# Performance work log

Measured on AMD Instinct MI355X. Metric: run time of the kernel, lower is better.

The kernel has to match this reference:

```python
import jax, jax.numpy as jnp
import numpy as np

N_NODES = 50000
N_EDGES = 800000
D_IN, D_HID, D_OUT = 128, 256, 128


def setup_inputs() -> dict:
    key = jax.random.key(0)
    ks = jax.random.split(key, 8)
    x = jax.random.normal(ks[0], (N_NODES, D_IN), dtype=jnp.float32)
    edge_index = jax.random.randint(ks[1], (2, N_EDGES), 0, N_NODES, dtype=jnp.int64)
    # Xavier-ish scale for stability
    W_l1 = jax.random.normal(ks[2], (D_HID, D_IN), dtype=jnp.float32) * (1.0 / np.sqrt(D_IN))
    b_l1 = jnp.zeros((D_HID,), dtype=jnp.float32)
    W_r1 = jax.random.normal(ks[3], (D_HID, D_IN), dtype=jnp.float32) * (1.0 / np.sqrt(D_IN))
    W_l2 = jax.random.normal(ks[4], (D_OUT, D_HID), dtype=jnp.float32) * (1.0 / np.sqrt(D_HID))
    b_l2 = jnp.zeros((D_OUT,), dtype=jnp.float32)
    W_r2 = jax.random.normal(ks[5], (D_OUT, D_HID), dtype=jnp.float32) * (1.0 / np.sqrt(D_HID))
    return {"x": x, "edge_index": edge_index, "W_l1": W_l1, "b_l1": b_l1,
            "W_r1": W_r1, "W_l2": W_l2, "b_l2": b_l2, "W_r2": W_r2}


def _sage_conv(x, src, dst, W_l, b_l, W_r):
    # SAGEConv (aggr='mean', root_weight=True, normalize=False):
    #   out_i = W_l @ mean_{j in N(i)} x_j + b_l + W_r @ x_i
    n = x.shape[0]
    msgs = x[src]                                             # [E, d] gather
    agg = jax.ops.segment_sum(msgs, dst, num_segments=n)      # [N, d] scatter-add
    deg = jax.ops.segment_sum(jnp.ones((src.shape[0],), x.dtype), dst,
                              num_segments=n)
    agg = agg / jnp.maximum(deg, 1.0)[:, None]                # mean (0 for isolated)
    return agg @ W_l.T + b_l + x @ W_r.T


def reference(x, edge_index, W_l1, b_l1, W_r1, W_l2, b_l2, W_r2):
    # Note: PyG BasicGNN with num_layers=1 and jk=None applies NO activation
    # after its single conv, so the stack is two bare SAGEConv layers.
    src, dst = edge_index[0], edge_index[1]
    h = _sage_conv(x, src, dst, W_l1, b_l1, W_r1)
    out = _sage_conv(h, src, dst, W_l2, b_l2, W_r2)
    return out
```

## Files before the change

kernel.cpp:

```cpp
#include <hip/hip_runtime.h>

typedef __attribute__((ext_vector_type(4))) float f32x4;
typedef __attribute__((ext_vector_type(8))) short bf16x8;

__device__ inline ushort f2bf(float f) {
    uint u = __builtin_bit_cast(uint, f);
    u += 0x7fff + ((u >> 16) & 1);
    return (ushort)(u >> 16);
}
__device__ inline float bf2f(ushort h) {
    uint u = ((uint)h) << 16;
    return __builtin_bit_cast(float, u);
}

#define GRP 8
#define NSLICE 6250
#define CHUNK 2048

__global__ __launch_bounds__(256) void k_hist_p(const int* __restrict__ ei,
                                                int* __restrict__ cnt, int nE) {
    const int g = blockIdx.x & 7;
    const int c = blockIdx.x >> 3;
    const int lo = g * NSLICE, hi = lo + NSLICE;
    #pragma unroll
    for (int p = 0; p < CHUNK / 256; ++p) {
        int e = c * CHUNK + p * 256 + threadIdx.x;
        if (e < nE) {
            int d = ei[nE + e];
            if (d >= lo && d < hi) atomicAdd(&cnt[d], 1);
        }
    }
}

__global__ __launch_bounds__(1024) void k_scan1(const int* __restrict__ cnt,
                                                int* __restrict__ rp,
                                                int* __restrict__ bsum, int n) {
    __shared__ int buf[1024];
    const int tid = threadIdx.x;
    const int i = blockIdx.x * 1024 + tid;
    int v = (i < n) ? cnt[i] : 0;
    buf[tid] = v;
    __syncthreads();
    #pragma unroll
    for (int off = 1; off < 1024; off <<= 1) {
        int t = 0;
        if (tid >= off) t = buf[tid - off];
        __syncthreads();
        if (tid >= off) buf[tid] += t;
        __syncthreads();
    }
    if (i < n) rp[i] = buf[tid] - v;
    if (tid == 1023) bsum[blockIdx.x] = buf[1023];
}

__global__ void k_scan2(const int* __restrict__ bsum, int* __restrict__ bofs,
                        int* __restrict__ rp, int nb, int n) {
    if (threadIdx.x == 0 && blockIdx.x == 0) {
        int run = 0;
        for (int b = 0; b < nb; ++b) { bofs[b] = run; run += bsum[b]; }
        rp[n] = run;
    }
}

__global__ __launch_bounds__(1024) void k_scan3(int* __restrict__ rp,
                                                const int* __restrict__ bofs, int n) {
    int i = blockIdx.x * 1024 + threadIdx.x;
    if (i < n) rp[i] += bofs[blockIdx.x];
}

__global__ __launch_bounds__(256) void k_fill_p(const int* __restrict__ ei,
                                                const int* __restrict__ rp,
                                                int* __restrict__ cur,
                                                int* __restrict__ srt, int nE) {
    const int g = blockIdx.x & 7;
    const int c = blockIdx.x >> 3;
    const int lo = g * NSLICE, hi = lo + NSLICE;
    #pragma unroll
    for (int p = 0; p < CHUNK / 256; ++p) {
        int e = c * CHUNK + p * 256 + threadIdx.x;
        if (e < nE) {
            int d = ei[nE + e];
            int s = ei[e];
            if (d >= lo && d < hi) {
                int pos = rp[d] + atomicAdd(&cur[d], 1);
                srt[pos] = s;
            }
        }
    }
}

__global__ __launch_bounds__(256) void k_cvt_x(const float* __restrict__ x,
                                               ushort* __restrict__ A1, int n) {
    int e4 = blockIdx.x * 256 + threadIdx.x;
    if (e4 >= n * 32) return;
    int i = e4 >> 5, c4 = e4 & 31;
    float4 v = *(const float4*)(x + (size_t)i * 128 + c4 * 4);
    ushort4 o;
    o.x = f2bf(v.x); o.y = f2bf(v.y); o.z = f2bf(v.z); o.w = f2bf(v.w);
    *(ushort4*)(A1 + (size_t)i * 256 + 128 + c4 * 4) = o;
}

__global__ __launch_bounds__(256) void k_cvt_w(
    const float* __restrict__ Wl1, const float* __restrict__ Wr1,
    const float* __restrict__ Wl2, const float* __restrict__ Wr2,
    ushort* __restrict__ W1cat, ushort* __restrict__ W2cat) {
    int t = blockIdx.x * 256 + threadIdx.x;
    int which = t >> 14;
    int r = (t >> 6) & 255;
    int kq = t & 63;
    const float* src;
    ushort* dst;
    if (which == 0) {
        src = (kq < 32) ? (Wl1 + (size_t)r * 128 + kq * 4)
                        : (Wr1 + (size_t)r * 128 + (kq - 32) * 4);
        dst = W1cat + (size_t)r * 256 + kq * 4;
    } else {
        src = (r < 128) ? (Wl2 + (size_t)r * 256 + kq * 4)
                        : (Wr2 + (size_t)(r - 128) * 256 + kq * 4);
        dst = W2cat + (size_t)r * 256 + kq * 4;
    }
    float4 v = *(const float4*)src;
    ushort4 o;
    o.x = f2bf(v.x); o.y = f2bf(v.y); o.z = f2bf(v.z); o.w = f2bf(v.w);
    *(ushort4*)dst = o;
}

__global__ __launch_bounds__(256) void k_gather1(ushort* A1,
                                                 const int* __restrict__ srt,
                                                 const int* __restrict__ rp, int n) {
    const int node = blockIdx.x * 4 + (threadIdx.x >> 6);
    if (node >= n) return;
    const int lane = threadIdx.x & 63;
    const int beg = rp[node], end = rp[node + 1];
    float ax = 0.f, ay = 0.f;
    int e = beg;
    for (; e + 7 < end; e += 8) {
        uint v[8];
        #pragma unroll
        for (int q = 0; q < 8; ++q)
            v[q] = *(const uint*)(A1 + (size_t)srt[e + q] * 256 + 128 + lane * 2);
        #pragma unroll
        for (int q = 0; q < 8; ++q) {
            ax += bf2f((ushort)v[q]);
            ay += bf2f((ushort)(v[q] >> 16));
        }
    }
    for (; e < end; ++e) {
        uint v0 = *(const uint*)(A1 + (size_t)srt[e] * 256 + 128 + lane * 2);
        ax += bf2f((ushort)v0);
        ay += bf2f((ushort)(v0 >> 16));
    }
    const float invd = 1.0f / fmaxf((float)(end - beg), 1.0f);
    uint o = ((uint)f2bf(ay * invd) << 16) | (uint)f2bf(ax * invd);
    *(uint*)(A1 + (size_t)node * 256 + lane * 2) = o;
}

__global__ __launch_bounds__(256) void k_gather2(const ushort* __restrict__ H2,
                                                 const int* __restrict__ srt,
                                                 const int* __restrict__ rp,
                                                 const float* __restrict__ b2,
                                                 float* __restrict__ out, int n) {
    const int node = blockIdx.x * 4 + (threadIdx.x >> 6);
    if (node >= n) return;
    const int lane = threadIdx.x & 63;
    const int beg = rp[node], end = rp[node + 1];
    float ax = 0.f, ay = 0.f;
    int e = beg;
    for (; e + 7 < end; e += 8) {
        uint v[8];
        #pragma unroll
        for (int q = 0; q < 8; ++q)
            v[q] = *(const uint*)(H2 + (size_t)srt[e + q] * 256 + lane * 2);
        #pragma unroll
        for (int q = 0; q < 8; ++q) {
            ax += bf2f((ushort)v[q]);
            ay += bf2f((ushort)(v[q] >> 16));
        }
    }
    for (; e < end; ++e) {
        uint v0 = *(const uint*)(H2 + (size_t)srt[e] * 256 + lane * 2);
        ax += bf2f((ushort)v0);
        ay += bf2f((ushort)(v0 >> 16));
    }
    const float invd = 1.0f / fmaxf((float)(end - beg), 1.0f);
    uint rv = *(const uint*)(H2 + (size_t)node * 256 + 128 + lane * 2);
    float2 bb = *(const float2*)(b2 + lane * 2);
    float2 res;
    res.x = ax * invd + bf2f((ushort)rv) + bb.x;
    res.y = ay * invd + bf2f((ushort)(rv >> 16)) + bb.y;
    *(float2*)(out + (size_t)node * 128 + lane * 2) = res;
}

__global__ __launch_bounds__(512, 4) void k_gemm_fused(
    const ushort* __restrict__ A, const ushort* __restrict__ W1,
    const ushort* __restrict__ W2, const float* __restrict__ b1,
    ushort* __restrict__ O, int n)
{
    __shared__ __align__(16) char sA[32768];
    __shared__ __align__(16) char sH[32768];
    const int bi = blockIdx.x * 64;
    const int tid = threadIdx.x;

    #pragma unroll
    for (int p = 0; p < 4; ++p) {
        const int o = p * 8192 + tid * 16;
        const int row = o >> 9;
        const int cb = o & 511;
        uint4 v = *(const uint4*)((const char*)A + (size_t)(bi + row) * 512 + cb);
        *(uint4*)(sA + row * 512 + (cb ^ ((row & 7) << 4))) = v;
    }
    __syncthreads();

    const int wid = tid >> 6;
    const int lane = tid & 63;
    const int wn = wid * 32;
    const int lr = lane & 15;
    const int lkb = (lane >> 4) * 16;
    const int crow0 = (lane >> 4) * 4;
    const int ccol = lane & 15;

    {
        f32x4 acc[4][2] = {};
        #pragma unroll
        for (int kk = 0; kk < 8; ++kk) {
            bf16x8 wf[2], af[4];
            #pragma unroll
            for (int ni = 0; ni < 2; ++ni)
                wf[ni] = *(const bf16x8*)((const char*)W1 + (size_t)(wn + ni * 16 + lr) * 512 + kk * 64 + lkb);
            #pragma unroll
            for (int mi = 0; mi < 4; ++mi) {
                const int row = mi * 16 + lr;
                af[mi] = *(const bf16x8*)(sA + row * 512 + ((kk * 64 + lkb) ^ ((row & 7) << 4)));
            }
            #pragma unroll
            for (int mi = 0; mi < 4; ++mi)
                #pragma unroll
                for (int ni = 0; ni < 2; ++ni)
                    acc[mi][ni] = __builtin_amdgcn_mfma_f32_16x16x32_bf16(
                        af[mi], wf[ni], acc[mi][ni], 0, 0, 0);
        }
        const float badd0 = b1[wn + ccol];
        const float badd1 = b1[wn + 16 + ccol];
        #pragma unroll
        for (int mi = 0; mi < 4; ++mi)
            #pragma unroll
            for (int ni = 0; ni < 2; ++ni) {
                const int col = wn + ni * 16 + ccol;
                const float badd = ni ? badd1 : badd0;
                #pragma unroll
                for (int j = 0; j < 4; ++j) {
                    const int row = mi * 16 + crow0 + j;
                    *(ushort*)(sH + row * 512 + ((col * 2) ^ ((row & 7) << 4))) =
                        f2bf(acc[mi][ni][j] + badd);
                }
            }
    }
    __syncthreads();

    {
        f32x4 acc[4][2] = {};
        #pragma unroll
        for (int kk = 0; kk < 8; ++kk) {
            bf16x8 wf[2], af[4];
            #pragma unroll
            for (int ni = 0; ni < 2; ++ni)
                wf[ni] = *(const bf16x8*)((const char*)W2 + (size_t)(wn + ni * 16 + lr) * 512 + kk * 64 + lkb);
            #pragma unroll
            for (int mi = 0; mi < 4; ++mi) {
                const int row = mi * 16 + lr;
                af[mi] = *(const bf16x8*)(sH + row * 512 + ((kk * 64 + lkb) ^ ((row & 7) << 4)));
            }
            #pragma unroll
            for (int mi = 0; mi < 4; ++mi)
                #pragma unroll
                for (int ni = 0; ni < 2; ++ni)
                    acc[mi][ni] = __builtin_amdgcn_mfma_f32_16x16x32_bf16(
                        af[mi], wf[ni], acc[mi][ni], 0, 0, 0);
        }
        #pragma unroll
        for (int mi = 0; mi < 4; ++mi)
            #pragma unroll
            for (int ni = 0; ni < 2; ++ni) {
                const int ocol = wn + ni * 16 + ccol;
                #pragma unroll
                for (int j = 0; j < 4; ++j) {
                    const int grow = bi + mi * 16 + crow0 + j;
                    if (grow < n)
                        O[(size_t)grow * 256 + ocol] = f2bf(acc[mi][ni][j]);
                }
            }
    }
}

extern "C" void kernel_launch(void* const* d_in, const int* in_sizes, int n_in,
                              void* d_out, int out_size, void* d_ws, size_t ws_size,
                              hipStream_t stream) {
    const float* x   = (const float*)d_in[0];
    const int*   ei  = (const int*)  d_in[1];
    const float* Wl1 = (const float*)d_in[2];
    const float* bl1 = (const float*)d_in[3];
    const float* Wr1 = (const float*)d_in[4];
    const float* Wl2 = (const float*)d_in[5];
    const float* bl2 = (const float*)d_in[6];
    const float* Wr2 = (const float*)d_in[7];
    float* out = (float*)d_out;

    const int nN = 50000;
    const int nE = in_sizes[1] / 2;

    char* ws = (char*)d_ws;
    int*    rp    = (int*)   (ws);
    int*    cnt   = (int*)   (ws + 262144);
    int*    cur   = (int*)   (ws + 524288);
    int*    bsum  = (int*)   (ws + 786432);
    int*    bofs  = (int*)   (ws + 790528);
    int*    srt   = (int*)   (ws + (size_t)1 * (1 << 20));
    ushort* W1cat = (ushort*)(ws + (size_t)5 * (1 << 20));
    ushort* W2cat = (ushort*)(ws + (size_t)5 * (1 << 20) + 256 * 1024);
    ushort* A1    = (ushort*)(ws + (size_t)6 * (1 << 20));
    ushort* H2    = (ushort*)(ws + (size_t)32 * (1 << 20));

    const int nb = (nN + 1023) / 1024;
    const int nChunks = (nE + CHUNK - 1) / CHUNK;

    hipMemsetAsync(ws + 262144, 0, 462144, stream);
    k_hist_p<<<nChunks * GRP, 256, 0, stream>>>(ei, cnt, nE);
    k_scan1<<<nb, 1024, 0, stream>>>(cnt, rp, bsum, nN);
    k_scan2<<<1, 64, 0, stream>>>(bsum, bofs, rp, nb, nN);
    k_scan3<<<nb, 1024, 0, stream>>>(rp, bofs, nN);
    k_fill_p<<<nChunks * GRP, 256, 0, stream>>>(ei, rp, cur, srt, nE);

    k_cvt_x<<<(nN * 32 + 255) / 256, 256, 0, stream>>>(x, A1, nN);
    k_cvt_w<<<128, 256, 0, stream>>>(Wl1, Wr1, Wl2, Wr2, W1cat, W2cat);

    k_gather1<<<(nN + 3) / 4, 256, 0, stream>>>(A1, srt, rp, nN);
    k_gemm_fused<<<(nN + 63) / 64, 512, 0, stream>>>(A1, W1cat, W2cat, bl1, H2, nN);

    k_gather2<<<(nN + 3) / 4, 256, 0, stream>>>(H2, srt, rp, bl2, out, nN);
}
```

Baseline: 294.5 us.

## Bucket CSR edges by source slice and gather 8 nodes per wave in lockstep

Splits each destination's neighbor list into 8 sub-buckets keyed by source-node slice, so the CSR is built over N*8 keys. The gather kernels then process 8 destination nodes per wavefront and walk all of them through the same source slice together. The goal is better L2 locality for the random row gathers and more loads in flight per wave. It also parallelizes the block-sum scan across a wavefront and merges the two conversion kernels into one launch. The cost is an 8x larger count/scan array, extra scan work, and divergent per-node loops inside each wave.

```diff
diff --git a/kernel.cpp b/kernel.cpp
--- a/kernel.cpp
+++ b/kernel.cpp
@@ -18,7 +18,7 @@
 #define CHUNK 2048
 
 __global__ __launch_bounds__(256) void k_hist_p(const int* __restrict__ ei,
-                                                int* __restrict__ cnt, int nE) {
+                                                int* __restrict__ cnt8, int nE) {
     const int g = blockIdx.x & 7;
     const int c = blockIdx.x >> 3;
     const int lo = g * NSLICE, hi = lo + NSLICE;
@@ -27,7 +27,8 @@
         int e = c * CHUNK + p * 256 + threadIdx.x;
         if (e < nE) {
             int d = ei[nE + e];
-            if (d >= lo && d < hi) atomicAdd(&cnt[d], 1);
+            int s = ei[e];
+            if (d >= lo && d < hi) atomicAdd(&cnt8[d * 8 + s / NSLICE], 1);
         }
     }
 }
@@ -55,11 +56,21 @@
 
 __global__ void k_scan2(const int* __restrict__ bsum, int* __restrict__ bofs,
                         int* __restrict__ rp, int nb, int n) {
-    if (threadIdx.x == 0 && blockIdx.x == 0) {
-        int run = 0;
-        for (int b = 0; b < nb; ++b) { bofs[b] = run; run += bsum[b]; }
-        rp[n] = run;
-    }
+    const int lane = threadIdx.x & 63;
+    int carry = 0;
+    for (int c = 0; c * 64 < nb; ++c) {
+        int i = c * 64 + lane;
+        int v = (i < nb) ? bsum[i] : 0;
+        int s = v;
+        #pragma unroll
+        for (int off = 1; off < 64; off <<= 1) {
+            int t = __shfl_up(s, off, 64);
+            if (lane >= off) s += t;
+        }
+        if (i < nb) bofs[i] = carry + s - v;
+        carry += __shfl(s, 63, 64);
+    }
+    if (lane == 0) rp[n] = carry;
 }
 
 __global__ __launch_bounds__(1024) void k_scan3(int* __restrict__ rp,
@@ -69,8 +80,8 @@
 }
 
 __global__ __launch_bounds__(256) void k_fill_p(const int* __restrict__ ei,
-                                                const int* __restrict__ rp,
-                                                int* __restrict__ cur,
+                                                const int* __restrict__ rp8,
+                                                int* __restrict__ cur8,
                                                 int* __restrict__ srt, int nE) {
     const int g = blockIdx.x & 7;
     const int c = blockIdx.x >> 3;
@@ -82,29 +93,34 @@
             int d = ei[nE + e];
             int s = ei[e];
             if (d >= lo && d < hi) {
-                int pos = rp[d] + atomicAdd(&cur[d], 1);
+                int k = d * 8 + s / NSLICE;
+                int pos = rp8[k] + atomicAdd(&cur8[k], 1);
                 srt[pos] = s;
             }
         }
     }
 }
 
-__global__ __launch_bounds__(256) void k_cvt_x(const float* __restrict__ x,
-                                               ushort* __restrict__ A1, int n) {
-    int e4 = blockIdx.x * 256 + threadIdx.x;
-    if (e4 >= n * 32) return;
-    int i = e4 >> 5, c4 = e4 & 31;
-    float4 v = *(const float4*)(x + (size_t)i * 128 + c4 * 4);
-    ushort4 o;
-    o.x = f2bf(v.x); o.y = f2bf(v.y); o.z = f2bf(v.z); o.w = f2bf(v.w);
-    *(ushort4*)(A1 + (size_t)i * 256 + 128 + c4 * 4) = o;
-}
-
-__global__ __launch_bounds__(256) void k_cvt_w(
-    const float* __restrict__ Wl1, const float* __restrict__ Wr1,
-    const float* __restrict__ Wl2, const float* __restrict__ Wr2,
-    ushort* __restrict__ W1cat, ushort* __restrict__ W2cat) {
-    int t = blockIdx.x * 256 + threadIdx.x;
+__global__ __launch_bounds__(256) void k_cvt(const float* __restrict__ x,
+                                             const float* __restrict__ Wl1,
+                                             const float* __restrict__ Wr1,
+                                             const float* __restrict__ Wl2,
+                                             const float* __restrict__ Wr2,
+                                             ushort* __restrict__ A1,
+                                             ushort* __restrict__ W1cat,
+                                             ushort* __restrict__ W2cat, int n) {
+    const int nxb = (n * 32 + 255) / 256;
+    if (blockIdx.x < nxb) {
+        int e4 = blockIdx.x * 256 + threadIdx.x;
+        if (e4 >= n * 32) return;
+        int i = e4 >> 5, c4 = e4 & 31;
+        float4 v = *(const float4*)(x + (size_t)i * 128 + c4 * 4);
+        ushort4 o;
+        o.x = f2bf(v.x); o.y = f2bf(v.y); o.z = f2bf(v.z); o.w = f2bf(v.w);
+        *(ushort4*)(A1 + (size_t)i * 256 + 128 + c4 * 4) = o;
+        return;
+    }
+    int t = (blockIdx.x - nxb) * 256 + threadIdx.x;
     int which = t >> 14;
     int r = (t >> 6) & 255;
     int kq = t & 63;
@@ -127,68 +143,114 @@
 
 __global__ __launch_bounds__(256) void k_gather1(ushort* A1,
                                                  const int* __restrict__ srt,
-                                                 const int* __restrict__ rp, int n) {
-    const int node = blockIdx.x * 4 + (threadIdx.x >> 6);
-    if (node >= n) return;
+                                                 const int* __restrict__ rp8, int n) {
+    const int wav = blockIdx.x * 4 + (threadIdx.x >> 6);
+    const int base = wav * 8;
+    if (base >= n) return;
     const int lane = threadIdx.x & 63;
-    const int beg = rp[node], end = rp[node + 1];
-    float ax = 0.f, ay = 0.f;
-    int e = beg;
-    for (; e + 7 < end; e += 8) {
-        uint v[8];
-        #pragma unroll
-        for (int q = 0; q < 8; ++q)
-            v[q] = *(const uint*)(A1 + (size_t)srt[e + q] * 256 + 128 + lane * 2);
+    float ax[8] = {}, ay[8] = {};
+    int deg[8] = {};
+    int curq[8], endq[8];
+    #pragma unroll
+    for (int q = 0; q < 8; ++q)
+        curq[q] = (base + q < n) ? rp8[(base + q) * 8] : 0;
+
+    #pragma unroll
+    for (int p = 0; p < 8; ++p) {
         #pragma unroll
         for (int q = 0; q < 8; ++q) {
-            ax += bf2f((ushort)v[q]);
-            ay += bf2f((ushort)(v[q] >> 16));
-        }
-    }
-    for (; e < end; ++e) {
-        uint v0 = *(const uint*)(A1 + (size_t)srt[e] * 256 + 128 + lane * 2);
-        ax += bf2f((ushort)v0);
-        ay += bf2f((ushort)(v0 >> 16));
-    }
-    const float invd = 1.0f / fmaxf((float)(end - beg), 1.0f);
-    uint o = ((uint)f2bf(ay * invd) << 16) | (uint)f2bf(ax * invd);
-    *(uint*)(A1 + (size_t)node * 256 + lane * 2) = o;
+            endq[q] = (base + q < n) ? rp8[(base + q) * 8 + p + 1] : 0;
+            deg[q] += endq[q] - curq[q];
+        }
+        bool any = true;
+        while (any) {
+            any = false;
+            uint v[8]; bool live[8];
+            #pragma unroll
+            for (int q = 0; q < 8; ++q) {
+                live[q] = curq[q] < endq[q];
+                if (live[q]) {
+                    int s = srt[curq[q]++];
+                    v[q] = *(const uint*)(A1 + (size_t)s * 256 + 128 + lane * 2);
+                    any = true;
+                }
+            }
+            #pragma unroll
+            for (int q = 0; q < 8; ++q)
+                if (live[q]) {
+                    ax[q] += bf2f((ushort)v[q]);
+                    ay[q] += bf2f((ushort)(v[q] >> 16));
+                }
+        }
+    }
+    #pragma unroll
+    for (int q = 0; q < 8; ++q) {
+        const int node = base + q;
+        if (node < n) {
+            const float invd = 1.0f / fmaxf((float)deg[q], 1.0f);
+            uint o = ((uint)f2bf(ay[q] * invd) << 16) | (uint)f2bf(ax[q] * invd);
+            *(uint*)(A1 + (size_t)node * 256 + lane * 2) = o;
+        }
+    }
 }
 
 __global__ __launch_bounds__(256) void k_gather2(const ushort* __restrict__ H2,
                                                  const int* __restrict__ srt,
-                                                 const int* __restrict__ rp,
+                                                 const int* __restrict__ rp8,
                                                  const float* __restrict__ b2,
                                                  float* __restrict__ out, int n) {
-    const int node = blockIdx.x * 4 + (threadIdx.x >> 6);
-    if (node >= n) return;
+    const int wav = blockIdx.x * 4 + (threadIdx.x >> 6);
+    const int base = wav * 8;
+    if (base >= n) return;
     const int lane = threadIdx.x & 63;
-    const int beg = rp[node], end = rp[node + 1];
-    float ax = 0.f, ay = 0.f;
-    int e = beg;
-    for (; e + 7 < end; e += 8) {
-        uint v[8];
-        #pragma unroll
-        for (int q = 0; q < 8; ++q)
-            v[q] = *(const uint*)(H2 + (size_t)srt[e + q] * 256 + lane * 2);
+    float ax[8] = {}, ay[8] = {};
+    int deg[8] = {};
+    int curq[8], endq[8];
+    #pragma unroll
+    for (int q = 0; q < 8; ++q)
+        curq[q] = (base + q < n) ? rp8[(base + q) * 8] : 0;
+
+    #pragma unroll
+    for (int p = 0; p < 8; ++p) {
         #pragma unroll
         for (int q = 0; q < 8; ++q) {
-            ax += bf2f((ushort)v[q]);
-            ay += bf2f((ushort)(v[q] >> 16));
-        }
-    }
-    for (; e < end; ++e) {
-        uint v0 = *(const uint*)(H2 + (size_t)srt[e] * 256 + lane * 2);
-        ax += bf2f((ushort)v0);
-        ay += bf2f((ushort)(v0 >> 16));
-    }
-    const float invd = 1.0f / fmaxf((float)(end - beg), 1.0f);
-    uint rv = *(const uint*)(H2 + (size_t)node * 256 + 128 + lane * 2);
+            endq[q] = (base + q < n) ? rp8[(base + q) * 8 + p + 1] : 0;
+            deg[q] += endq[q] - curq[q];
+        }
+        bool any = true;
+        while (any) {
+            any = false;
+            uint v[8]; bool live[8];
+            #pragma unroll
+            for (int q = 0; q < 8; ++q) {
+                live[q] = curq[q] < endq[q];
+                if (live[q]) {
+                    int s = srt[curq[q]++];
+                    v[q] = *(const uint*)(H2 + (size_t)s * 256 + lane * 2);
+                    any = true;
+                }
+            }
+            #pragma unroll
+            for (int q = 0; q < 8; ++q)
+                if (live[q]) {
+                    ax[q] += bf2f((ushort)v[q]);
+                    ay[q] += bf2f((ushort)(v[q] >> 16));
+                }
+        }
+    }
     float2 bb = *(const float2*)(b2 + lane * 2);
-    float2 res;
-    res.x = ax * invd + bf2f((ushort)rv) + bb.x;
-    res.y = ay * invd + bf2f((ushort)(rv >> 16)) + bb.y;
-    *(float2*)(out + (size_t)node * 128 + lane * 2) = res;
+    #pragma unroll
+    for (int q = 0; q < 8; ++q) {
+        const int node = base + q;
+        if (node < n) {
+            const float invd = 1.0f / fmaxf((float)deg[q], 1.0f);
+            uint rv = *(const uint*)(H2 + (size_t)node * 256 + 128 + lane * 2);
+            float2 res;
+            res.x = ax[q] * invd + bf2f((ushort)rv) + bb.x;
+            res.y = ay[q] * invd + bf2f((ushort)(rv >> 16)) + bb.y;
+            *(float2*)(out + (size_t)node * 128 + lane * 2) = res;
+        }
+    }
 }
 
 __global__ __launch_bounds__(512, 4) void k_gemm_fused(
@@ -307,34 +369,35 @@
 
     const int nN = 50000;
     const int nE = in_sizes[1] / 2;
+    const int n8 = nN * 8;
 
     char* ws = (char*)d_ws;
-    int*    rp    = (int*)   (ws);
-    int*    cnt   = (int*)   (ws + 262144);
-    int*    cur   = (int*)   (ws + 524288);
-    int*    bsum  = (int*)   (ws + 786432);
-    int*    bofs  = (int*)   (ws + 790528);
-    int*    srt   = (int*)   (ws + (size_t)1 * (1 << 20));
-    ushort* W1cat = (ushort*)(ws + (size_t)5 * (1 << 20));
-    ushort* W2cat = (ushort*)(ws + (size_t)5 * (1 << 20) + 256 * 1024);
-    ushort* A1    = (ushort*)(ws + (size_t)6 * (1 << 20));
-    ushort* H2    = (ushort*)(ws + (size_t)32 * (1 << 20));
-
-    const int nb = (nN + 1023) / 1024;
+    int*    rp8   = (int*)   (ws);
+    int*    cnt8  = (int*)   (ws + (size_t)2 * (1 << 20));
+    int*    cur8  = (int*)   (ws + (size_t)2 * (1 << 20) + 1600000);
+    int*    bsum  = (int*)   (ws + (size_t)6 * (1 << 20));
+    int*    bofs  = (int*)   (ws + (size_t)6 * (1 << 20) + 4096);
+    int*    srt   = (int*)   (ws + (size_t)7 * (1 << 20));
+    ushort* W1cat = (ushort*)(ws + (size_t)11 * (1 << 20));
+    ushort* W2cat = (ushort*)(ws + (size_t)11 * (1 << 20) + 262144);
+    ushort* A1    = (ushort*)(ws + (size_t)12 * (1 << 20));
+    ushort* H2    = (ushort*)(ws + (size_t)38 * (1 << 20));
+
+    const int nb8 = (n8 + 1023) / 1024;
     const int nChunks = (nE + CHUNK - 1) / CHUNK;
-
-    hipMemsetAsync(ws + 262144, 0, 462144, stream);
-    k_hist_p<<<nChunks * GRP, 256, 0, stream>>>(ei, cnt, nE);
-    k_scan1<<<nb, 1024, 0, stream>>>(cnt, rp, bsum, nN);
-    k_scan2<<<1, 64, 0, stream>>>(bsum, bofs, rp, nb, nN);
-    k_scan3<<<nb, 1024, 0, stream>>>(rp, bofs, nN);
-    k_fill_p<<<nChunks * GRP, 256, 0, stream>>>(ei, rp, cur, srt, nE);
-
-    k_cvt_x<<<(nN * 32 + 255) / 256, 256, 0, stream>>>(x, A1, nN);
-    k_cvt_w<<<128, 256, 0, stream>>>(Wl1, Wr1, Wl2, Wr2, W1cat, W2cat);
-
-    k_gather1<<<(nN + 3) / 4, 256, 0, stream>>>(A1, srt, rp, nN);
+    const int nxb = (nN * 32 + 255) / 256;
+
+    hipMemsetAsync(cnt8, 0, (size_t)2 * 1600000, stream);
+    k_hist_p<<<nChunks * GRP, 256, 0, stream>>>(ei, cnt8, nE);
+    k_scan1<<<nb8, 1024, 0, stream>>>(cnt8, rp8, bsum, n8);
+    k_scan2<<<1, 64, 0, stream>>>(bsum, bofs, rp8, nb8, n8);
+    k_scan3<<<nb8, 1024, 0, stream>>>(rp8, bofs, n8);
+    k_fill_p<<<nChunks * GRP, 256, 0, stream>>>(ei, rp8, cur8, srt, nE);
+
+    k_cvt<<<nxb + 128, 256, 0, stream>>>(x, Wl1, Wr1, Wl2, Wr2, A1, W1cat, W2cat, nN);
+
+    k_gather1<<<(nN + 31) / 32, 256, 0, stream>>>(A1, srt, rp8, nN);
     k_gemm_fused<<<(nN + 63) / 64, 512, 0, stream>>>(A1, W1cat, W2cat, bl1, H2, nN);
 
-    k_gather2<<<(nN + 3) / 4, 256, 0, stream>>>(H2, srt, rp, bl2, out, nN);
-}
+    k_gather2<<<(nN + 31) / 32, 256, 0, stream>>>(H2, srt, rp8, bl2, out, nN);
+}
```

Result: slower. 668.4 us (+127.0%).
